# Performance work log

Hardware: AMD Instinct MI355X
Metric: run time of the kernel (lower is better)

Reference implementation:

```python
import jax, jax.numpy as jnp
import numpy as np

B, S, H = 4, 4096, 256
NH, W = 8, 128
DH = H // NH
FF = 1024
NEG = -1e9

def gelu(x):
    return jax.nn.gelu(x, approximate=False)

def layer_norm(x, g, b, eps=1e-9):
    # torch .std() is unbiased (ddof=1); note the (std + eps) denominator, not sqrt(var+eps)
    mean = jnp.mean(x, axis=-1, keepdims=True)
    std = jnp.std(x, axis=-1, keepdims=True, ddof=1)
    return g * (x - mean) / (std + eps) + b

def causal_conv(x, w, b, dilation):
    # x: (B,S,C), w: (9, Cin, Cout); left-padded causal conv (Conv class)
    pad = dilation * 8
    y = jax.lax.conv_general_dilated(x, w, window_strides=(1,), padding=[(pad, 0)],
                                     rhs_dilation=(dilation,), dimension_numbers=('NWC', 'WIO', 'NWC'))
    return y + b

def sliding_window_attention(q, k, v, bias):
    # q,k,v: (B,NH,S,DH); q pre-scaled. Faithful to Longformer sliding_chunks_matmul_qk/pv:
    # band of 2W+1 relative offsets per query, out-of-range keys masked to -inf before softmax.
    b, h, s, d = q.shape
    c = s // W  # number of length-W query chunks
    qc = q.reshape(b, h, c, W, d)
    kp = jnp.pad(k, ((0, 0), (0, 0), (W, W), (0, 0)))
    vp = jnp.pad(v, ((0, 0), (0, 0), (W, W), (0, 0)))
    kidx = (jnp.arange(c) * W)[:, None] + jnp.arange(3 * W)[None, :]  # (c,3W) overlapping key chunks
    kc = kp[:, :, kidx, :]  # (b,h,c,3W,d)
    vc = vp[:, :, kidx, :]
    scores = jnp.einsum('bhcxd,bhcyd->bhcxy', qc, kc)  # (b,h,c,W,3W)
    x = jnp.arange(W)
    r = jnp.arange(2 * W + 1)
    band_idx = x[:, None] + r[None, :]  # (W,2W+1), values in [0,3W-1]
    band = jnp.take_along_axis(scores, band_idx[None, None, None], axis=-1)  # (b,h,c,W,2W+1)
    i = jnp.arange(s).reshape(c, W)
    j = i[:, :, None] + (r - W)[None, None, :]  # global key index per band entry
    valid = (j >= 0) & (j < s)
    band = jnp.where(valid[None, None], band + bias, NEG)  # relative bias depends only on offset
    probs = jax.nn.softmax(band.astype(jnp.float32), axis=-1).astype(q.dtype)
    ridx = jnp.arange(3 * W)[None, :] - x[:, None]  # (W,3W) inverse band->chunk map
    vmask = ((ridx >= 0) & (ridx <= 2 * W)).astype(probs.dtype)
    pc = jnp.take_along_axis(probs, jnp.clip(ridx, 0, 2 * W)[None, None, None], axis=-1) * vmask[None, None, None]
    return jnp.einsum('bhcxy,bhcyd->bhcxd', pc, vc).reshape(b, h, s, d)


def setup_inputs() -> dict:
    key = jax.random.key(0)
    ks = jax.random.split(key, 12)
    inputs = jax.random.normal(ks[0], (B, S, H), jnp.float32)
    dw_w = jax.random.normal(ks[1], (9,), jnp.float32) * 0.1   # depthwise (9,1) kernel, 1 channel
    dw_b = jnp.zeros((1,), jnp.float32)
    pw_w = jax.random.normal(ks[2], (3,), jnp.float32) * 0.5   # pointwise 1->3 conv (scalars)
    pw_b = jnp.zeros((3,), jnp.float32)
    Wq = jax.random.normal(ks[3], (H, H), jnp.float32) * 0.02
    Wk = jax.random.normal(ks[4], (H, H), jnp.float32) * 0.02
    Wv = jax.random.normal(ks[5], (H, H), jnp.float32) * 0.02
    Wo = jax.random.normal(ks[6], (H, H), jnp.float32) * 0.02
    rel_bias = jax.random.normal(ks[7], (2 * S,), jnp.float32) * 0.02
    ln1_g = jnp.ones((H,), jnp.float32); ln1_b = jnp.zeros((H,), jnp.float32)
    ln2_g = jnp.ones((H,), jnp.float32); ln2_b = jnp.zeros((H,), jnp.float32)
    w1 = jax.random.normal(ks[8], (9, H, FF), jnp.float32) * 0.02
    b1 = jnp.zeros((FF,), jnp.float32)
    w2 = jax.random.normal(ks[9], (9, FF, H), jnp.float32) * 0.02
    b2 = jnp.zeros((H,), jnp.float32)
    return {"inputs": inputs, "dw_w": dw_w, "dw_b": dw_b, "pw_w": pw_w, "pw_b": pw_b,
            "Wq": Wq, "Wk": Wk, "Wv": Wv, "Wo": Wo, "rel_bias": rel_bias,
            "ln1_g": ln1_g, "ln1_b": ln1_b, "ln2_g": ln2_g, "ln2_b": ln2_b,
            "w1": w1, "b1": b1, "w2": w2, "b2": b2}


def reference(inputs, dw_w, dw_b, pw_w, pw_b, Wq, Wk, Wv, Wo, rel_bias,
              ln1_g, ln1_b, ln2_g, ln2_b, w1, b1, w2, b2):
    x = inputs
    xn = layer_norm(x, ln1_g, ln1_b)
    # SepConv2d QKV generator: depthwise (9,1) conv along seq (shared over features), GELU,
    # pointwise 1x1 conv 1->3 channels, then GELU again (self.relu in MHA.forward)
    xp = jnp.pad(xn, ((0, 0), (4, 4), (0, 0)))
    dw = jnp.zeros_like(xn)
    for t in range(9):
        dw = dw + dw_w[t] * xp[:, t:t + S, :]
    dw = dw + dw_b[0]
    hmid = gelu(dw)
    qkv = gelu(hmid[None] * pw_w.reshape(3, 1, 1, 1) + pw_b.reshape(3, 1, 1, 1))  # (3,B,S,H)
    q = qkv[0] @ Wq
    k = qkv[1] @ Wk
    v = qkv[2] @ Wv
    split = lambda t: t.reshape(B, S, NH, DH).transpose(0, 2, 1, 3)
    q, k, v = split(q), split(k), split(v)
    q = q * (DH ** -0.5)
    # relative_position_index = arange(2W+1).repeat(lens,1) -> bias uses table[:2W+1] per offset
    bias = rel_bias[:2 * W + 1]
    ctx = sliding_window_attention(q, k, v, bias)
    ctx = ctx.transpose(0, 2, 1, 3).reshape(B, S, H)
    x = x + ctx @ Wo
    xn2 = layer_norm(x, ln2_g, ln2_b)
    # PositionwiseFeedForward 'cc': causal dilated convs; GELU applied after every layer (incl. last)
    f = gelu(causal_conv(xn2, w1, b1, 1))
    f = gelu(causal_conv(f, w2, b2, 8))
    return x + f
```

## Files before the change

### kernel.cpp

```cpp
#include <hip/hip_runtime.h>
#include <stdint.h>

typedef uint16_t u16;
typedef uint32_t u32;

typedef __attribute__((ext_vector_type(8))) short bf16x8;
typedef __attribute__((ext_vector_type(4))) float f32x4;

typedef __attribute__((address_space(1))) const u32 gas_u32;
typedef __attribute__((address_space(3))) u32 las_u32;

#define S_LEN 4096
#define HDIM  256
#define FFDIM 1024

__device__ __forceinline__ float bf2f(u16 u) { return __uint_as_float(((u32)u) << 16); }
__device__ __forceinline__ u16 f2bf(float f) {
  u32 x = __float_as_uint(f);
  return (u16)((x + 0x7fffu + ((x >> 16) & 1u)) >> 16);
}
__device__ __forceinline__ float gelu_f(float x) {
  return 0.5f * x * (1.0f + erff(x * 0.7071067811865475f));
}
__device__ __forceinline__ void glds16(const u16* g, u16* l) {
  __builtin_amdgcn_global_load_lds((gas_u32*)g, (las_u32*)l, 16, 0, 0);
}

__global__ __launch_bounds__(256) void front_kernel(
    const float* __restrict__ Wq, const float* __restrict__ Wk, const float* __restrict__ Wv,
    const float* __restrict__ Wo, const float* __restrict__ W1, const float* __restrict__ W2,
    u16* __restrict__ WqT, u16* __restrict__ WkT, u16* __restrict__ WvT,
    u16* __restrict__ WoT, u16* __restrict__ W1T, u16* __restrict__ W2T, float qscale,
    const float* __restrict__ X, u16* __restrict__ gq, u16* __restrict__ gk, u16* __restrict__ gv,
    const float* __restrict__ ln1g, const float* __restrict__ ln1b,
    const float* __restrict__ dw_w, const float* __restrict__ dw_b,
    const float* __restrict__ pw_w, const float* __restrict__ pw_b) {
  __shared__ u16 t[32][33];
  __shared__ float xnl[24 * 256];
  const int bid = blockIdx.x;
  const int tid = threadIdx.x;
  if (bid < 4864) {
    const float* in; u16* out; int K, N; float scale = 1.0f; int idx;
    if (bid < 256) {
      K = 256; N = 256; idx = bid & 63;
      const int w = bid >> 6;
      in = (w == 0) ? Wq : (w == 1) ? Wk : (w == 2) ? Wv : Wo;
      out = (w == 0) ? WqT : (w == 1) ? WkT : (w == 2) ? WvT : WoT;
      if (w == 0) scale = qscale;
    } else if (bid < 2560) {
      K = 2304; N = 1024; idx = bid - 256; in = W1; out = W1T;
    } else {
      K = 9216; N = 256; idx = bid - 2560; in = W2; out = W2T;
    }
    const int kt = K >> 5;
    const int k0 = (idx % kt) * 32, n0 = (idx / kt) * 32;
    const int tx = tid & 31, ty = tid >> 5;
#pragma unroll
    for (int i = ty; i < 32; i += 8) t[i][tx] = f2bf(in[(long)(k0 + i) * N + (n0 + tx)] * scale);
    __syncthreads();
#pragma unroll
    for (int i = ty; i < 32; i += 8) out[(long)(n0 + i) * K + (k0 + tx)] = t[tx][i];
    return;
  }
  const int ro = (bid - 4864) * 16;
  const int seg_lo = ro & ~(S_LEN - 1);
  const int lane = tid & 63;
  const int ri = tid >> 6;
  const int c0 = lane * 4;
#pragma unroll
  for (int p = 0; p < 6; ++p) {
    const int h = ro - 4 + p * 4 + ri;
    float y[4] = {0.f, 0.f, 0.f, 0.f};
    if (h >= seg_lo && h < seg_lo + S_LEN) {
      float4 f = *(const float4*)(X + (long)h * HDIM + c0);
      float v[4] = {f.x, f.y, f.z, f.w};
      float s = v[0] + v[1] + v[2] + v[3];
#pragma unroll
      for (int o = 32; o > 0; o >>= 1) s += __shfl_xor(s, o);
      const float mean = s * (1.0f / 256.0f);
      float ss = 0.f;
#pragma unroll
      for (int j = 0; j < 4; ++j) { float d = v[j] - mean; ss += d * d; }
#pragma unroll
      for (int o = 32; o > 0; o >>= 1) ss += __shfl_xor(ss, o);
      const float inv_ = 1.0f / (sqrtf(ss * (1.0f / 255.0f)) + 1e-9f);
#pragma unroll
      for (int j = 0; j < 4; ++j) y[j] = ln1g[c0 + j] * (v[j] - mean) * inv_ + ln1b[c0 + j];
    }
    float4 o_; o_.x = y[0]; o_.y = y[1]; o_.z = y[2]; o_.w = y[3];
    *(float4*)&xnl[(p * 4 + ri) * 256 + c0] = o_;
  }
  __syncthreads();
  const float b0 = dw_b[0];
  float wv[9];
#pragma unroll
  for (int q = 0; q < 9; ++q) wv[q] = dw_w[q];
  const float pwv[3] = {pw_w[0], pw_w[1], pw_w[2]};
  const float pbv[3] = {pw_b[0], pw_b[1], pw_b[2]};
  u16* outs[3] = {gq, gk, gv};
#pragma unroll
  for (int p = 0; p < 4; ++p) {
    const int lrow = p * 4 + ri;
    float a0 = b0, a1 = b0, a2 = b0, a3 = b0;
#pragma unroll
    for (int q = 0; q < 9; ++q) {
      const float w = wv[q];
      float4 xv = *(const float4*)&xnl[(lrow + q) * 256 + c0];
      a0 = fmaf(w, xv.x, a0); a1 = fmaf(w, xv.y, a1);
      a2 = fmaf(w, xv.z, a2); a3 = fmaf(w, xv.w, a3);
    }
    float h[4];
    h[0] = gelu_f(a0); h[1] = gelu_f(a1); h[2] = gelu_f(a2); h[3] = gelu_f(a3);
    const long orow = (long)(ro + lrow);
#pragma unroll
    for (int pp = 0; pp < 3; ++pp) {
      float y[4];
#pragma unroll
      for (int j = 0; j < 4; ++j) y[j] = gelu_f(fmaf(h[j], pwv[pp], pbv[pp]));
      uint2 o_;
      o_.x = (u32)f2bf(y[0]) | ((u32)f2bf(y[1]) << 16);
      o_.y = (u32)f2bf(y[2]) | ((u32)f2bf(y[3]) << 16);
      *(uint2*)(outs[pp] + orow * HDIM + c0) = o_;
    }
  }
}

__global__ __launch_bounds__(256) void ln2_kernel(const float* __restrict__ inv, u16* __restrict__ outv,
                                                  const float* __restrict__ g, const float* __restrict__ bsh,
                                                  uint4* __restrict__ gx, uint4* __restrict__ gf) {
  const int tid = threadIdx.x;
  if (blockIdx.x >= 4096) {
    int t = (blockIdx.x - 4096) * 256 + tid;
    const uint4 z = {0u, 0u, 0u, 0u};
    if (t < 1024) {
      const int s = t >> 8, o = t & 255;
      gx[(long)s * 131328 + o] = z;
    } else {
      t -= 1024;
      if (t < 32768) {
        const int s = t >> 13, o = t & 8191;
        gf[(long)s * 532480 + o] = z;
      }
    }
    return;
  }
  const int lane = tid & 63;
  const long row = (long)blockIdx.x * 4 + (tid >> 6);
  const int c0 = lane * 4;
  float v[4];
  float4 f = *(const float4*)(inv + row * HDIM + c0);
  v[0] = f.x; v[1] = f.y; v[2] = f.z; v[3] = f.w;
  float s = v[0] + v[1] + v[2] + v[3];
#pragma unroll
  for (int o = 32; o > 0; o >>= 1) s += __shfl_xor(s, o);
  const float mean = s * (1.0f / 256.0f);
  float ss = 0.f;
#pragma unroll
  for (int j = 0; j < 4; ++j) { float d = v[j] - mean; ss += d * d; }
#pragma unroll
  for (int o = 32; o > 0; o >>= 1) ss += __shfl_xor(ss, o);
  const float inv_ = 1.0f / (sqrtf(ss * (1.0f / 255.0f)) + 1e-9f);
  float y[4];
#pragma unroll
  for (int j = 0; j < 4; ++j) y[j] = g[c0 + j] * (v[j] - mean) * inv_ + bsh[c0 + j];
  const long orow = (row >> 12) * 4104 + 8 + (row & (S_LEN - 1));
  uint2 o_;
  o_.x = (u32)f2bf(y[0]) | ((u32)f2bf(y[1]) << 16);
  o_.y = (u32)f2bf(y[2]) | ((u32)f2bf(y[3]) << 16);
  *(uint2*)(outv + orow * HDIM + c0) = o_;
}

__global__ __launch_bounds__(256) void gemm_qkv(
    const u16* __restrict__ A, const u16* __restrict__ BT, u16* __restrict__ Outv,
    u16* __restrict__ vt, int KW, int N, long a_z, long b_z, long o_z) {
  __shared__ __align__(16) u16 As[128 * 64];
  __shared__ __align__(16) u16 Bs[128 * 64];
  const int tid = threadIdx.x;
  const int lane = tid & 63;
  const int wid = tid >> 6;
  const int wm = (wid & 1) * 64;
  const int wn = (wid >> 1) * 64;
  const int fm = lane & 15;
  const int fq = lane >> 4;
  const int t0 = blockIdx.x * 128;
  const int n0 = blockIdx.y * 128;
  A += (long)blockIdx.z * a_z;
  BT += (long)blockIdx.z * b_z;

  const int srow = lane >> 3;
  const int cseg = (((lane & 7) ^ srow) << 3);

  f32x4 acc[4][4];
#pragma unroll
  for (int a = 0; a < 4; ++a)
#pragma unroll
    for (int b = 0; b < 4; ++b) acc[a][b] = (f32x4){0.f, 0.f, 0.f, 0.f};

  u16* alb = &As[wid * 32 * 64];
  u16* blb = &Bs[wid * 32 * 64];

  for (int k0 = 0; k0 < KW; k0 += 64) {
    const u16* ag = A + (long)(t0 + wid * 32 + srow) * KW + k0 + cseg;
    const u16* bg = BT + (long)(n0 + wid * 32 + srow) * KW + k0 + cseg;
#pragma unroll
    for (int j = 0; j < 4; ++j) {
      glds16(ag + (long)(8 * j) * KW, alb + j * 8 * 64);
      glds16(bg + (long)(8 * j) * KW, blb + j * 8 * 64);
    }
    __syncthreads();
#pragma unroll
    for (int kk = 0; kk < 2; ++kk) {
      const int g = kk * 4 + fq;
      const u16* ap = &As[(wm + fm) * 64 + ((g ^ (fm & 7)) << 3)];
      const u16* bp = &Bs[(wn + fm) * 64 + ((g ^ (fm & 7)) << 3)];
      bf16x8 af[4], bfv[4];
#pragma unroll
      for (int t = 0; t < 4; ++t) {
        af[t] = *(const bf16x8*)(ap + t * 1024);
        bfv[t] = *(const bf16x8*)(bp + t * 1024);
      }
#pragma unroll
      for (int mi = 0; mi < 4; ++mi)
#pragma unroll
        for (int ni = 0; ni < 4; ++ni)
          acc[mi][ni] = __builtin_amdgcn_mfma_f32_16x16x32_bf16(af[mi], bfv[ni], acc[mi][ni], 0, 0, 0);
    }
    __syncthreads();
  }

#pragma unroll
  for (int mi = 0; mi < 4; ++mi)
#pragma unroll
    for (int ni = 0; ni < 4; ++ni) {
      if (blockIdx.z == 2) {
        const int col = n0 + wn + ni * 16 + fm;
        const int hh = col >> 5, dd = col & 31;
        const long trow0 = t0 + wm + mi * 16 + fq * 4;
        const long bb = trow0 >> 12;
        const int s0 = (int)(trow0 & (S_LEN - 1));
        uint2 o_;
        o_.x = (u32)f2bf(acc[mi][ni][0]) | ((u32)f2bf(acc[mi][ni][1]) << 16);
        o_.y = (u32)f2bf(acc[mi][ni][2]) | ((u32)f2bf(acc[mi][ni][3]) << 16);
        *(uint2*)(vt + ((bb * 8 + hh) * 32 + dd) * S_LEN + s0) = o_;
      } else {
#pragma unroll
        for (int r = 0; r < 4; ++r) {
          const long trow = t0 + wm + mi * 16 + fq * 4 + r;
          const int col = n0 + wn + ni * 16 + fm;
          (Outv + (long)blockIdx.z * o_z)[trow * N + col] = f2bf(acc[mi][ni][r]);
        }
      }
    }
}

__global__ __launch_bounds__(256) void gemm_wo(
    const u16* __restrict__ A, const u16* __restrict__ BT, float* __restrict__ Outv,
    const float* __restrict__ residv, int KW, int N) {
  __shared__ __align__(16) u16 As[128 * 64];
  __shared__ __align__(16) u16 Bs[128 * 64];
  const int tid = threadIdx.x;
  const int lane = tid & 63;
  const int wid = tid >> 6;
  const int wm = (wid & 1) * 64;
  const int wn = (wid >> 1) * 64;
  const int fm = lane & 15;
  const int fq = lane >> 4;
  const int t0 = blockIdx.x * 128;
  const int n0 = blockIdx.y * 128;

  const int srow = lane >> 3;
  const int cseg = (((lane & 7) ^ srow) << 3);

  f32x4 acc[4][4];
#pragma unroll
  for (int a = 0; a < 4; ++a)
#pragma unroll
    for (int b = 0; b < 4; ++b) acc[a][b] = (f32x4){0.f, 0.f, 0.f, 0.f};

  u16* alb = &As[wid * 32 * 64];
  u16* blb = &Bs[wid * 32 * 64];

  for (int k0 = 0; k0 < KW; k0 += 64) {
    const u16* ag = A + (long)(t0 + wid * 32 + srow) * KW + k0 + cseg;
    const u16* bg = BT + (long)(n0 + wid * 32 + srow) * KW + k0 + cseg;
#pragma unroll
    for (int j = 0; j < 4; ++j) {
      glds16(ag + (long)(8 * j) * KW, alb + j * 8 * 64);
      glds16(bg + (long)(8 * j) * KW, blb + j * 8 * 64);
    }
    __syncthreads();
#pragma unroll
    for (int kk = 0; kk < 2; ++kk) {
      const int g = kk * 4 + fq;
      const u16* ap = &As[(wm + fm) * 64 + ((g ^ (fm & 7)) << 3)];
      const u16* bp = &Bs[(wn + fm) * 64 + ((g ^ (fm & 7)) << 3)];
      bf16x8 af[4], bfv[4];
#pragma unroll
      for (int t = 0; t < 4; ++t) {
        af[t] = *(const bf16x8*)(ap + t * 1024);
        bfv[t] = *(const bf16x8*)(bp + t * 1024);
      }
#pragma unroll
      for (int mi = 0; mi < 4; ++mi)
#pragma unroll
        for (int ni = 0; ni < 4; ++ni)
          acc[mi][ni] = __builtin_amdgcn_mfma_f32_16x16x32_bf16(af[mi], bfv[ni], acc[mi][ni], 0, 0, 0);
    }
    __syncthreads();
  }

#pragma unroll
  for (int mi = 0; mi < 4; ++mi)
#pragma unroll
    for (int ni = 0; ni < 4; ++ni)
#pragma unroll
      for (int r = 0; r < 4; ++r) {
        const long trow = t0 + wm + mi * 16 + fq * 4 + r;
        const int col = n0 + wn + ni * 16 + fm;
        Outv[trow * N + col] = acc[mi][ni][r] + residv[trow * N + col];
      }
}

__global__ __launch_bounds__(256) void attn_mfma(const u16* __restrict__ Q, const u16* __restrict__ K,
                                                 const u16* __restrict__ VT, const float* __restrict__ rel,
                                                 u16* __restrict__ CTX) {
  __shared__ __align__(16) u16 Ks[384 * 36];
  __shared__ __align__(16) u16 VTs[32 * 388];
  __shared__ __align__(16) u16 Ps[4][32 * 72];
  __shared__ float bias_s[260];
  const int c = blockIdx.x, h = blockIdx.y, b = blockIdx.z;
  const int tid = threadIdx.x;
  const int lane = tid & 63, wid = tid >> 6;
  const int fm = lane & 15, fq = lane >> 4;
  const int j0 = c * 128 - 128;
  const long kvbase = ((long)b * S_LEN) * HDIM + h * 32;
  const long vtbase = (((long)b * 8 + h) * 32) * S_LEN;

  for (int idx = tid; idx < 384 * 4; idx += 256) {
    const int jj = idx >> 2, seg = (idx & 3) * 8;
    int j = j0 + jj; j = j < 0 ? 0 : (j > S_LEN - 1 ? S_LEN - 1 : j);
    uint4 kv = *(const uint4*)(K + kvbase + (long)j * HDIM + seg);
    *(uint4*)&Ks[jj * 36 + seg] = kv;
  }
#pragma unroll
  for (int p = 0; p < 6; ++p) {
    const int idx = p * 256 + tid;
    const int d = idx / 48, seg = idx - d * 48;
    int off = j0 + seg * 8; off = off < 0 ? 0 : (off > S_LEN - 8 ? S_LEN - 8 : off);
    uint4 vv = *(const uint4*)(VT + vtbase + (long)d * S_LEN + off);
    *(uint4*)&VTs[d * 388 + seg * 8] = vv;
  }
  for (int idx = tid; idx < 257; idx += 256) bias_s[idx] = rel[idx];
  __syncthreads();

  bf16x8 aq[2];
#pragma unroll
  for (int mi = 0; mi < 2; ++mi)
    aq[mi] = *(const bf16x8*)(Q + kvbase + (long)(c * 128 + wid * 32 + mi * 16 + fm) * HDIM + fq * 8);

  const int klo = (c == 0) ? 128 : 0;
  const int khi = (c == 31) ? 255 : 383;

  float m_r[2][4], l_r[2][4];
  f32x4 acc[2][2];
#pragma unroll
  for (int mi = 0; mi < 2; ++mi)
#pragma unroll
    for (int r = 0; r < 4; ++r) { m_r[mi][r] = -1e9f; l_r[mi][r] = 0.f; }
#pragma unroll
  for (int mi = 0; mi < 2; ++mi)
#pragma unroll
    for (int nd = 0; nd < 2; ++nd) acc[mi][nd] = (f32x4){0.f, 0.f, 0.f, 0.f};

  u16* pw = &Ps[wid][0];

  for (int ch = 0; ch < 6; ++ch) {
    f32x4 sc[2][4];
#pragma unroll
    for (int ni = 0; ni < 4; ++ni) {
      bf16x8 bk = *(const bf16x8*)&Ks[(ch * 64 + ni * 16 + fm) * 36 + fq * 8];
#pragma unroll
      for (int mi = 0; mi < 2; ++mi)
        sc[mi][ni] = __builtin_amdgcn_mfma_f32_16x16x32_bf16(aq[mi], bk, (f32x4){0.f, 0.f, 0.f, 0.f}, 0, 0, 0);
    }
    float cm[2][4];
#pragma unroll
    for (int mi = 0; mi < 2; ++mi)
#pragma unroll
      for (int r = 0; r < 4; ++r) cm[mi][r] = -1e9f;
#pragma unroll
    for (int mi = 0; mi < 2; ++mi)
#pragma unroll
      for (int ni = 0; ni < 4; ++ni) {
        const int keyloc = ch * 64 + ni * 16 + fm;
        const bool kval = (keyloc >= klo) && (keyloc <= khi);
#pragma unroll
        for (int r = 0; r < 4; ++r) {
          const int qloc = wid * 32 + mi * 16 + fq * 4 + r;
          const int rr = keyloc - qloc;
          const bool valid = kval && (rr >= 0) && (rr <= 256);
          const int rc = valid ? rr : 0;
          float vv = sc[mi][ni][r] + bias_s[rc];
          vv = valid ? vv : -1e9f;
          sc[mi][ni][r] = vv;
          cm[mi][r] = fmaxf(cm[mi][r], vv);
        }
      }
#pragma unroll
    for (int mi = 0; mi < 2; ++mi)
#pragma unroll
      for (int r = 0; r < 4; ++r) {
        float x = cm[mi][r];
        x = fmaxf(x, __shfl_xor(x, 1));
        x = fmaxf(x, __shfl_xor(x, 2));
        x = fmaxf(x, __shfl_xor(x, 4));
        x = fmaxf(x, __shfl_xor(x, 8));
        cm[mi][r] = x;
      }
    float alpha[2][4];
#pragma unroll
    for (int mi = 0; mi < 2; ++mi)
#pragma unroll
      for (int r = 0; r < 4; ++r) {
        const float nm = fmaxf(m_r[mi][r], cm[mi][r]);
        alpha[mi][r] = __expf(m_r[mi][r] - nm);
        m_r[mi][r] = nm;
        l_r[mi][r] *= alpha[mi][r];
      }
#pragma unroll
    for (int mi = 0; mi < 2; ++mi)
#pragma unroll
      for (int nd = 0; nd < 2; ++nd)
#pragma unroll
        for (int r = 0; r < 4; ++r) acc[mi][nd][r] *= alpha[mi][r];
#pragma unroll
    for (int mi = 0; mi < 2; ++mi)
#pragma unroll
      for (int ni = 0; ni < 4; ++ni)
#pragma unroll
        for (int r = 0; r < 4; ++r) {
          const float pv = __expf(sc[mi][ni][r] - m_r[mi][r]);
          l_r[mi][r] += pv;
          pw[(mi * 16 + fq * 4 + r) * 72 + ni * 16 + fm] = f2bf(pv);
        }
#pragma unroll
    for (int kc = 0; kc < 2; ++kc) {
      bf16x8 ap[2], bv[2];
#pragma unroll
      for (int mi = 0; mi < 2; ++mi)
        ap[mi] = *(const bf16x8*)&pw[(mi * 16 + fm) * 72 + kc * 32 + fq * 8];
#pragma unroll
      for (int nd = 0; nd < 2; ++nd)
        bv[nd] = *(const bf16x8*)&VTs[(nd * 16 + fm) * 388 + ch * 64 + kc * 32 + fq * 8];
#pragma unroll
      for (int mi = 0; mi < 2; ++mi)
#pragma unroll
        for (int nd = 0; nd < 2; ++nd)
          acc[mi][nd] = __builtin_amdgcn_mfma_f32_16x16x32_bf16(ap[mi], bv[nd], acc[mi][nd], 0, 0, 0);
    }
  }

  float linv[2][4];
#pragma unroll
  for (int mi = 0; mi < 2; ++mi)
#pragma unroll
    for (int r = 0; r < 4; ++r) {
      float x = l_r[mi][r];
      x += __shfl_xor(x, 1);
      x += __shfl_xor(x, 2);
      x += __shfl_xor(x, 4);
      x += __shfl_xor(x, 8);
      linv[mi][r] = 1.0f / x;
    }
#pragma unroll
  for (int mi = 0; mi < 2; ++mi)
#pragma unroll
    for (int nd = 0; nd < 2; ++nd)
#pragma unroll
      for (int r = 0; r < 4; ++r) {
        const long s = c * 128 + wid * 32 + mi * 16 + fq * 4 + r;
        CTX[((long)b * S_LEN + s) * HDIM + h * 32 + nd * 16 + fm] = f2bf(acc[mi][nd][r] * linv[mi][r]);
      }
}

template <int APITCH, int NTAPS, int DIL, int NN>
__global__ __launch_bounds__(256, 2) void gemm_conv(
    const u16* __restrict__ Apad, const u16* __restrict__ BT, void* __restrict__ Outv,
    const float* __restrict__ bias,
    int SEGR, int BPITCH, int OSEGR, int OGUARD) {
  constexpr int AROWS = 256 + (NTAPS - 1) * DIL;
  constexpr int AOPS = (AROWS + 7) / 8;
  __shared__ __align__(16) u16 As[AOPS * 8 * 64];
  __shared__ __align__(16) u16 Bs2[2][128 * 64];
  const int tid = threadIdx.x;
  const int lane = tid & 63;
  const int wid = tid >> 6;
  const int wm = (wid & 1) * 128;
  const int wn = (wid >> 1) * 64;
  const int fm = lane & 15;
  const int fq = lane >> 4;
  const int t0 = blockIdx.x * 256;
  const int n0 = blockIdx.y * 128;

  const int seg = t0 >> 12;
  const long abase = (long)seg * SEGR + (t0 & (S_LEN - 1));
  const int srow = lane >> 3;
  const int cseg = (((lane & 7) ^ srow) << 3);

  f32x4 acc[8][4];
#pragma unroll
  for (int a = 0; a < 8; ++a)
#pragma unroll
    for (int b = 0; b < 4; ++b) acc[a][b] = (f32x4){0.f, 0.f, 0.f, 0.f};

  for (int k0 = 0; k0 < APITCH; k0 += 64) {
    for (int op = wid; op < AOPS; op += 4)
      glds16(Apad + (abase + op * 8 + srow) * APITCH + k0 + cseg, &As[op * 8 * 64]);
#pragma unroll
    for (int j = 0; j < 4; ++j)
      glds16(BT + (long)(n0 + wid * 32 + j * 8 + srow) * BPITCH + k0 + cseg,
             &Bs2[0][(wid * 32 + j * 8) * 64]);
    __syncthreads();
#pragma unroll
    for (int u = 0; u < NTAPS; ++u) {
      if (u + 1 < NTAPS) {
        const long bc = (long)(u + 1) * APITCH + k0;
#pragma unroll
        for (int j = 0; j < 4; ++j)
          glds16(BT + (long)(n0 + wid * 32 + j * 8 + srow) * BPITCH + bc + cseg,
                 &Bs2[(u + 1) & 1][(wid * 32 + j * 8) * 64]);
      }
      const int du = u * DIL;
      const u16* bsp = Bs2[u & 1];
#pragma unroll
      for (int kk = 0; kk < 2; ++kk) {
        const int g = kk * 4 + fq;
        const u16* ap = &As[(wm + fm + du) * 64 + ((g ^ ((fm + du) & 7)) << 3)];
        const u16* bp = &bsp[(wn + fm) * 64 + ((g ^ (fm & 7)) << 3)];
        bf16x8 af[8], bfv[4];
#pragma unroll
        for (int t = 0; t < 8; ++t) af[t] = *(const bf16x8*)(ap + t * 1024);
#pragma unroll
        for (int t = 0; t < 4; ++t) bfv[t] = *(const bf16x8*)(bp + t * 1024);
#pragma unroll
        for (int mi = 0; mi < 8; ++mi)
#pragma unroll
          for (int ni = 0; ni < 4; ++ni)
            acc[mi][ni] = __builtin_amdgcn_mfma_f32_16x16x32_bf16(af[mi], bfv[ni], acc[mi][ni], 0, 0, 0);
      }
      __syncthreads();
    }
  }

#pragma unroll
  for (int mi = 0; mi < 8; ++mi)
#pragma unroll
    for (int ni = 0; ni < 4; ++ni)
#pragma unroll
      for (int r = 0; r < 4; ++r) {
        const long trow = t0 + wm + mi * 16 + fq * 4 + r;
        const int col = n0 + wn + ni * 16 + fm;
        const long orow = (trow >> 12) * OSEGR + OGUARD + (trow & (S_LEN - 1));
        ((u16*)Outv)[orow * NN + col] = f2bf(gelu_f(acc[mi][ni][r] + bias[col]));
      }
}

__global__ __launch_bounds__(256) void gemm_conv_s(
    const u16* __restrict__ Apad, const u16* __restrict__ BT, u16* __restrict__ Outv,
    int APITCH, int SEGR, int BPITCH, int ntaps, int dil, int N, long out_z_off) {
  __shared__ __align__(16) u16 As[144 * 64];
  __shared__ __align__(16) u16 Bs2[2][128 * 64];
  const int tid = threadIdx.x;
  const int lane = tid & 63;
  const int wid = tid >> 6;
  const int wm = (wid & 1) * 64;
  const int wn = (wid >> 1) * 64;
  const int fm = lane & 15;
  const int fq = lane >> 4;
  const int t0 = blockIdx.x * 128;
  const int n0 = blockIdx.y * 128;
  const int tap0 = blockIdx.z * ntaps;

  const int seg = t0 >> 12;
  const long abase = (long)seg * SEGR + (t0 & (S_LEN - 1)) + (long)tap0 * dil;
  const int aops = (128 + (ntaps - 1) * dil + 7) >> 3;

  const int srow = lane >> 3;
  const int cseg = (((lane & 7) ^ srow) << 3);

  f32x4 acc[4][4];
#pragma unroll
  for (int a = 0; a < 4; ++a)
#pragma unroll
    for (int b = 0; b < 4; ++b) acc[a][b] = (f32x4){0.f, 0.f, 0.f, 0.f};

  for (int k0 = 0; k0 < APITCH; k0 += 64) {
    for (int op = wid; op < aops; op += 4)
      glds16(Apad + (abase + op * 8 + srow) * APITCH + k0 + cseg, &As[op * 8 * 64]);
    {
      const long bc = (long)tap0 * APITCH + k0;
#pragma unroll
      for (int j = 0; j < 4; ++j)
        glds16(BT + (long)(n0 + wid * 32 + j * 8 + srow) * BPITCH + bc + cseg,
               &Bs2[0][(wid * 32 + j * 8) * 64]);
    }
    __syncthreads();
    for (int u = 0; u < ntaps; ++u) {
      if (u + 1 < ntaps) {
        const long bc = (long)(tap0 + u + 1) * APITCH + k0;
#pragma unroll
        for (int j = 0; j < 4; ++j)
          glds16(BT + (long)(n0 + wid * 32 + j * 8 + srow) * BPITCH + bc + cseg,
                 &Bs2[(u + 1) & 1][(wid * 32 + j * 8) * 64]);
      }
      const int du = u * dil;
      const u16* bsp = Bs2[u & 1];
#pragma unroll
      for (int kk = 0; kk < 2; ++kk) {
        const int g = kk * 4 + fq;
        const u16* ap = &As[(wm + fm + du) * 64 + ((g ^ (fm & 7)) << 3)];
        const u16* bp = &bsp[(wn + fm) * 64 + ((g ^ (fm & 7)) << 3)];
        bf16x8 af[4], bfv[4];
#pragma unroll
        for (int t = 0; t < 4; ++t) {
          af[t] = *(const bf16x8*)(ap + t * 1024);
          bfv[t] = *(const bf16x8*)(bp + t * 1024);
        }
#pragma unroll
        for (int mi = 0; mi < 4; ++mi)
#pragma unroll
          for (int ni = 0; ni < 4; ++ni)
            acc[mi][ni] = __builtin_amdgcn_mfma_f32_16x16x32_bf16(af[mi], bfv[ni], acc[mi][ni], 0, 0, 0);
      }
      __syncthreads();
    }
  }

#pragma unroll
  for (int mi = 0; mi < 4; ++mi)
#pragma unroll
    for (int ni = 0; ni < 4; ++ni)
#pragma unroll
      for (int r = 0; r < 4; ++r) {
        const long trow = t0 + wm + mi * 16 + fq * 4 + r;
        const int col = n0 + wn + ni * 16 + fm;
        (Outv + (long)blockIdx.z * out_z_off)[trow * N + col] = f2bf(acc[mi][ni][r]);
      }
}

__global__ __launch_bounds__(256) void final_kernel(const float* __restrict__ x2, const u16* __restrict__ P,
                                                    const float* __restrict__ b2, float* __restrict__ out) {
  const long i4 = ((long)blockIdx.x * 256 + threadIdx.x) * 4;
  const int c0 = (int)(i4 & (HDIM - 1));
  float4 xa = *(const float4*)(x2 + i4);
  uint2 u0 = *(const uint2*)(P + i4);
  uint2 u1 = *(const uint2*)(P + 4194304 + i4);
  uint2 u2 = *(const uint2*)(P + 8388608 + i4);
  float pv[4];
  pv[0] = bf2f((u16)(u0.x & 0xffffu)) + bf2f((u16)(u1.x & 0xffffu)) + bf2f((u16)(u2.x & 0xffffu));
  pv[1] = bf2f((u16)(u0.x >> 16)) + bf2f((u16)(u1.x >> 16)) + bf2f((u16)(u2.x >> 16));
  pv[2] = bf2f((u16)(u0.y & 0xffffu)) + bf2f((u16)(u1.y & 0xffffu)) + bf2f((u16)(u2.y & 0xffffu));
  pv[3] = bf2f((u16)(u0.y >> 16)) + bf2f((u16)(u1.y >> 16)) + bf2f((u16)(u2.y >> 16));
  float4 o_;
  o_.x = xa.x + gelu_f(pv[0] + b2[c0 + 0]);
  o_.y = xa.y + gelu_f(pv[1] + b2[c0 + 1]);
  o_.z = xa.z + gelu_f(pv[2] + b2[c0 + 2]);
  o_.w = xa.w + gelu_f(pv[3] + b2[c0 + 3]);
  *(float4*)(out + i4) = o_;
}

extern "C" void kernel_launch(void* const* d_in, const int* in_sizes, int n_in,
                              void* d_out, int out_size, void* d_ws, size_t ws_size,
                              hipStream_t stream) {
  (void)in_sizes; (void)n_in; (void)out_size;
  const float* X    = (const float*)d_in[0];
  const float* dw_w = (const float*)d_in[1];
  const float* dw_b = (const float*)d_in[2];
  const float* pw_w = (const float*)d_in[3];
  const float* pw_b = (const float*)d_in[4];
  const float* Wq   = (const float*)d_in[5];
  const float* Wk   = (const float*)d_in[6];
  const float* Wv   = (const float*)d_in[7];
  const float* Wo   = (const float*)d_in[8];
  const float* rel  = (const float*)d_in[9];
  const float* ln1g = (const float*)d_in[10];
  const float* ln1b = (const float*)d_in[11];
  const float* ln2g = (const float*)d_in[12];
  const float* ln2b = (const float*)d_in[13];
  const float* w1   = (const float*)d_in[14];
  const float* b1   = (const float*)d_in[15];
  const float* w2   = (const float*)d_in[16];
  const float* b2   = (const float*)d_in[17];

  if (ws_size < 119537664) return;

  char* ws = (char*)d_ws;
  u16* WqT = (u16*)(ws + 0);
  u16* WkT = (u16*)(ws + 131072);
  u16* WvT = (u16*)(ws + 262144);
  u16* WoT = (u16*)(ws + 393216);
  u16* W1T = (u16*)(ws + 524288);
  u16* W2T = (u16*)(ws + 5242880);
  float* x2  = (float*)(ws + 10485760);
  u16* gq  = (u16*)(ws + 27262976);
  u16* gk  = (u16*)(ws + 35651584);
  u16* gv  = (u16*)(ws + 44040192);
  u16* q   = (u16*)(ws + 52428800);
  u16* vt  = (u16*)(ws + 69206016);
  u16* ctx = (u16*)(ws + 77594624);
  u16* f1p  = (u16*)(ws + 27262976);
  u16* xn2p = (u16*)(ws + 61341696);
  u16* P    = (u16*)(ws + 61341696);

  const float qscale = 0.17677669529663687f;
  front_kernel<<<5888, 256, 0, stream>>>(Wq, Wk, Wv, Wo, w1, w2,
      WqT, WkT, WvT, WoT, W1T, W2T, qscale,
      X, gq, gk, gv, ln1g, ln1b, dw_w, dw_b, pw_w, pw_b);

  gemm_qkv<<<dim3(128, 2, 3), 256, 0, stream>>>(gq, WqT, q, vt,
      256, 256, 4194304, 65536, 4194304);

  attn_mfma<<<dim3(32, 8, 4), 256, 0, stream>>>(q, q + 4194304, vt, rel, ctx);

  gemm_wo<<<dim3(128, 2), 256, 0, stream>>>(ctx, WoT, x2, X, 256, 256);

  ln2_kernel<<<4228, 256, 0, stream>>>(x2, xn2p, ln2g, ln2b, (uint4*)xn2p, (uint4*)f1p);

  gemm_conv<256, 9, 1, 1024><<<dim3(64, 8), 256, 0, stream>>>(
      xn2p, W1T, f1p, b1, 4104, 2304, 4160, 64);

  gemm_conv_s<<<dim3(128, 2, 3), 256, 0, stream>>>(f1p, W2T, P,
      1024, 4160, 9216, 3, 8, 256, 4194304);

  final_kernel<<<4096, 256, 0, stream>>>(x2, P, b2, (float*)d_out);
}
```

Baseline: 381.8 us.

## Prepack conv weights in MFMA fragment order and stream B straight to registers

The front kernel now packs W1 and W2 into bf16 tiles already laid out as MFMA B-fragments, replacing the plain transposes. A new unified conv GEMM loads those fragments from global memory into registers with a one-iteration prefetch and double-buffers only the A tile in LDS, so B no longer goes through LDS. The second conv moves from a tap split with 128-row tiles to an input-channel split-K (4 partials) with 256-row tiles, and the final kernel now sums four partials. This aims to cut LDS traffic and barriers in the FFN GEMMs. In exchange it adds register pressure and extra partial-sum memory traffic.

Measured after the change: 385.2 us. About the same (+0.9%).

```diff
diff --git a/kernel.cpp b/kernel.cpp
--- a/kernel.cpp
+++ b/kernel.cpp
@@ -30,7 +30,7 @@
     const float* __restrict__ Wq, const float* __restrict__ Wk, const float* __restrict__ Wv,
     const float* __restrict__ Wo, const float* __restrict__ W1, const float* __restrict__ W2,
     u16* __restrict__ WqT, u16* __restrict__ WkT, u16* __restrict__ WvT,
-    u16* __restrict__ WoT, u16* __restrict__ W1T, u16* __restrict__ W2T, float qscale,
+    u16* __restrict__ WoT, u16* __restrict__ W1F, u16* __restrict__ W2F, float qscale,
     const float* __restrict__ X, u16* __restrict__ gq, u16* __restrict__ gk, u16* __restrict__ gv,
     const float* __restrict__ ln1g, const float* __restrict__ ln1b,
     const float* __restrict__ dw_w, const float* __restrict__ dw_b,
@@ -39,30 +39,48 @@
   __shared__ float xnl[24 * 256];
   const int bid = blockIdx.x;
   const int tid = threadIdx.x;
-  if (bid < 4864) {
-    const float* in; u16* out; int K, N; float scale = 1.0f; int idx;
-    if (bid < 256) {
-      K = 256; N = 256; idx = bid & 63;
-      const int w = bid >> 6;
-      in = (w == 0) ? Wq : (w == 1) ? Wk : (w == 2) ? Wv : Wo;
-      out = (w == 0) ? WqT : (w == 1) ? WkT : (w == 2) ? WvT : WoT;
-      if (w == 0) scale = qscale;
-    } else if (bid < 2560) {
-      K = 2304; N = 1024; idx = bid - 256; in = W1; out = W1T;
-    } else {
-      K = 9216; N = 256; idx = bid - 2560; in = W2; out = W2T;
-    }
-    const int kt = K >> 5;
-    const int k0 = (idx % kt) * 32, n0 = (idx / kt) * 32;
+  if (bid < 256) {
+    const int idx = bid & 63;
+    const int w = bid >> 6;
+    const float* in = (w == 0) ? Wq : (w == 1) ? Wk : (w == 2) ? Wv : Wo;
+    u16* out = (w == 0) ? WqT : (w == 1) ? WkT : (w == 2) ? WvT : WoT;
+    const float scale = (w == 0) ? qscale : 1.0f;
+    const int k0 = (idx & 7) * 32, n0 = (idx >> 3) * 32;
     const int tx = tid & 31, ty = tid >> 5;
 #pragma unroll
-    for (int i = ty; i < 32; i += 8) t[i][tx] = f2bf(in[(long)(k0 + i) * N + (n0 + tx)] * scale);
+    for (int i = ty; i < 32; i += 8) t[i][tx] = f2bf(in[(long)(k0 + i) * 256 + (n0 + tx)] * scale);
     __syncthreads();
 #pragma unroll
-    for (int i = ty; i < 32; i += 8) out[(long)(n0 + i) * K + (k0 + tx)] = t[tx][i];
+    for (int i = ty; i < 32; i += 8) out[(long)(n0 + i) * 256 + (k0 + tx)] = t[tx][i];
     return;
   }
-  const int ro = (bid - 4864) * 16;
+  if (bid < 1408) {
+    const int isC2 = bid >= 832;
+    const int idx = bid - (isC2 ? 832 : 256);
+    const float* w = isC2 ? W2 : W1;
+    u16* dst = isC2 ? W2F : W1F;
+    const int AP = isC2 ? 1024 : 256;
+    const int NNl = isC2 ? 256 : 1024;
+    const int per_n = (AP / 64) * 9;
+    const int n64g = idx / per_n;
+    const int r = idx - n64g * per_n;
+    const int k0i = r / 9, u = r - k0i * 9;
+    const long pktbase = (((long)n64g * (AP / 64) + k0i) * 9 + u) * 2;
+    for (int g = tid; g < 512; g += 256) {
+      const int kk = g >> 8, rr = g & 255, tt = rr >> 6, ln = rr & 63;
+      const int n = n64g * 64 + tt * 16 + (ln & 15);
+      const int kin = k0i * 64 + kk * 32 + (ln >> 4) * 8;
+      const float* src = w + (long)(u * AP + kin) * NNl + n;
+      u32 p0 = (u32)f2bf(src[0]) | ((u32)f2bf(src[(long)NNl]) << 16);
+      u32 p1 = (u32)f2bf(src[2l * NNl]) | ((u32)f2bf(src[3l * NNl]) << 16);
+      u32 p2 = (u32)f2bf(src[4l * NNl]) | ((u32)f2bf(src[5l * NNl]) << 16);
+      u32 p3 = (u32)f2bf(src[6l * NNl]) | ((u32)f2bf(src[7l * NNl]) << 16);
+      uint4 pk; pk.x = p0; pk.y = p1; pk.z = p2; pk.w = p3;
+      *(uint4*)(dst + (pktbase + kk) * 2048 + (long)(tt * 64 + ln) * 8) = pk;
+    }
+    return;
+  }
+  const int ro = (bid - 1408) * 16;
   const int seg_lo = ro & ~(S_LEN - 1);
   const int lane = tid & 63;
   const int ri = tid >> 6;
@@ -483,29 +501,25 @@
       }
 }
 
-template <int APITCH, int NTAPS, int DIL, int NN>
-__global__ __launch_bounds__(256, 2) void gemm_conv(
-    const u16* __restrict__ Apad, const u16* __restrict__ BT, void* __restrict__ Outv,
-    const float* __restrict__ bias,
-    int SEGR, int BPITCH, int OSEGR, int OGUARD) {
-  constexpr int AROWS = 256 + (NTAPS - 1) * DIL;
+template <int EPI, int APITCH, int DIL, int NN, int K0PERZ>
+__global__ __launch_bounds__(256, 2) void gemm_convB(
+    const u16* __restrict__ Apad, const u16* __restrict__ Bpk, void* __restrict__ Outv,
+    const float* __restrict__ bias, int SEGR, int OSEGR, int OGUARD, long out_z_off) {
+  constexpr int K0 = APITCH / 64;
+  constexpr int AROWS = 256 + 8 * DIL;
   constexpr int AOPS = (AROWS + 7) / 8;
-  __shared__ __align__(16) u16 As[AOPS * 8 * 64];
-  __shared__ __align__(16) u16 Bs2[2][128 * 64];
-  const int tid = threadIdx.x;
-  const int lane = tid & 63;
-  const int wid = tid >> 6;
-  const int wm = (wid & 1) * 128;
-  const int wn = (wid >> 1) * 64;
-  const int fm = lane & 15;
-  const int fq = lane >> 4;
-  const int t0 = blockIdx.x * 256;
-  const int n0 = blockIdx.y * 128;
-
+  __shared__ __align__(16) u16 As[2][AOPS * 8 * 64];
+  const int tid = threadIdx.x, lane = tid & 63, wid = tid >> 6;
+  const int wm = (wid & 1) * 128, wn = (wid >> 1) * 64;
+  const int fm = lane & 15, fq = lane >> 4;
+  const int t0 = blockIdx.x * 256, n0 = blockIdx.y * 128;
+  const int zz = blockIdx.z;
+  const int k0base = zz * K0PERZ;
   const int seg = t0 >> 12;
   const long abase = (long)seg * SEGR + (t0 & (S_LEN - 1));
   const int srow = lane >> 3;
   const int cseg = (((lane & 7) ^ srow) << 3);
+  const long n64g = (n0 + wn) >> 6;
 
   f32x4 acc[8][4];
 #pragma unroll
@@ -513,44 +527,67 @@
 #pragma unroll
     for (int b = 0; b < 4; ++b) acc[a][b] = (f32x4){0.f, 0.f, 0.f, 0.f};
 
-  for (int k0 = 0; k0 < APITCH; k0 += 64) {
-    for (int op = wid; op < AOPS; op += 4)
-      glds16(Apad + (abase + op * 8 + srow) * APITCH + k0 + cseg, &As[op * 8 * 64]);
-#pragma unroll
-    for (int j = 0; j < 4; ++j)
-      glds16(BT + (long)(n0 + wid * 32 + j * 8 + srow) * BPITCH + k0 + cseg,
-             &Bs2[0][(wid * 32 + j * 8) * 64]);
-    __syncthreads();
-#pragma unroll
-    for (int u = 0; u < NTAPS; ++u) {
-      if (u + 1 < NTAPS) {
-        const long bc = (long)(u + 1) * APITCH + k0;
-#pragma unroll
-        for (int j = 0; j < 4; ++j)
-          glds16(BT + (long)(n0 + wid * 32 + j * 8 + srow) * BPITCH + bc + cseg,
-                 &Bs2[(u + 1) & 1][(wid * 32 + j * 8) * 64]);
-      }
-      const int du = u * DIL;
-      const u16* bsp = Bs2[u & 1];
-#pragma unroll
-      for (int kk = 0; kk < 2; ++kk) {
-        const int g = kk * 4 + fq;
-        const u16* ap = &As[(wm + fm + du) * 64 + ((g ^ ((fm + du) & 7)) << 3)];
-        const u16* bp = &bsp[(wn + fm) * 64 + ((g ^ (fm & 7)) << 3)];
-        bf16x8 af[8], bfv[4];
-#pragma unroll
-        for (int t = 0; t < 8; ++t) af[t] = *(const bf16x8*)(ap + t * 1024);
-#pragma unroll
-        for (int t = 0; t < 4; ++t) bfv[t] = *(const bf16x8*)(bp + t * 1024);
-#pragma unroll
-        for (int mi = 0; mi < 8; ++mi)
-#pragma unroll
-          for (int ni = 0; ni < 4; ++ni)
-            acc[mi][ni] = __builtin_amdgcn_mfma_f32_16x16x32_bf16(af[mi], bfv[ni], acc[mi][ni], 0, 0, 0);
-      }
-      __syncthreads();
-    }
-  }
+#define STAGE_A(k0i, buf)                                                              \
+  {                                                                                    \
+    const int kc_ = (k0base + (k0i)) * 64;                                             \
+    for (int op = wid; op < AOPS; op += 4)                                             \
+      glds16(Apad + (abase + op * 8 + srow) * APITCH + kc_ + cseg, &As[(buf)][op * 8 * 64]); \
+  }
+
+#define LOAD_B(it, dst)                                                                \
+  {                                                                                    \
+    const int k0i_ = (it) / 9, u_ = (it) - k0i_ * 9;                                   \
+    const u16* pb_ = Bpk + (((n64g * K0 + (k0base + k0i_)) * 9 + u_) * 2) * 2048 + (long)lane * 8; \
+    _Pragma("unroll")                                                                  \
+    for (int kk_ = 0; kk_ < 2; ++kk_)                                                  \
+      _Pragma("unroll")                                                                \
+      for (int t_ = 0; t_ < 4; ++t_)                                                   \
+        dst[kk_ * 4 + t_] = *(const bf16x8*)(pb_ + kk_ * 2048 + t_ * 512);             \
+  }
+
+#define MFMA_TAP(u, buf, br)                                                           \
+  {                                                                                    \
+    const int du_ = (u) * DIL;                                                         \
+    _Pragma("unroll")                                                                  \
+    for (int kk_ = 0; kk_ < 2; ++kk_) {                                                \
+      const int g_ = kk_ * 4 + fq;                                                     \
+      const u16* ap_ = &As[(buf)][(wm + fm + du_) * 64 + ((g_ ^ ((fm + du_) & 7)) << 3)]; \
+      bf16x8 af_[8];                                                                   \
+      _Pragma("unroll")                                                                \
+      for (int t_ = 0; t_ < 8; ++t_) af_[t_] = *(const bf16x8*)(ap_ + t_ * 1024);      \
+      _Pragma("unroll")                                                                \
+      for (int mi_ = 0; mi_ < 8; ++mi_)                                                \
+        _Pragma("unroll")                                                              \
+        for (int ni_ = 0; ni_ < 4; ++ni_)                                              \
+          acc[mi_][ni_] = __builtin_amdgcn_mfma_f32_16x16x32_bf16(af_[mi_], br[kk_ * 4 + ni_], acc[mi_][ni_], 0, 0, 0); \
+    }                                                                                  \
+  }
+
+  constexpr int NIT = K0PERZ * 9;
+  bf16x8 br0[8], br1[8];
+  STAGE_A(0, 0);
+  LOAD_B(0, br0);
+  __syncthreads();
+  for (int it = 0; it < NIT; it += 2) {
+    {
+      const int k0i = it / 9, u = it - k0i * 9;
+      if (it + 1 < NIT) LOAD_B(it + 1, br1);
+      if (u == 1 && k0i + 1 < K0PERZ) STAGE_A(k0i + 1, (k0i + 1) & 1);
+      MFMA_TAP(u, k0i & 1, br0);
+      if (u == 8) __syncthreads();
+    }
+    {
+      const int it2 = it + 1;
+      const int k0i = it2 / 9, u = it2 - k0i * 9;
+      if (it2 + 1 < NIT) LOAD_B(it2 + 1, br0);
+      if (u == 1 && k0i + 1 < K0PERZ) STAGE_A(k0i + 1, (k0i + 1) & 1);
+      MFMA_TAP(u, k0i & 1, br1);
+      if (u == 8) __syncthreads();
+    }
+  }
+#undef STAGE_A
+#undef LOAD_B
+#undef MFMA_TAP
 
 #pragma unroll
   for (int mi = 0; mi < 8; ++mi)
@@ -560,91 +597,13 @@
       for (int r = 0; r < 4; ++r) {
         const long trow = t0 + wm + mi * 16 + fq * 4 + r;
         const int col = n0 + wn + ni * 16 + fm;
-        const long orow = (trow >> 12) * OSEGR + OGUARD + (trow & (S_LEN - 1));
-        ((u16*)Outv)[orow * NN + col] = f2bf(gelu_f(acc[mi][ni][r] + bias[col]));
-      }
-}
-
-__global__ __launch_bounds__(256) void gemm_conv_s(
-    const u16* __restrict__ Apad, const u16* __restrict__ BT, u16* __restrict__ Outv,
-    int APITCH, int SEGR, int BPITCH, int ntaps, int dil, int N, long out_z_off) {
-  __shared__ __align__(16) u16 As[144 * 64];
-  __shared__ __align__(16) u16 Bs2[2][128 * 64];
-  const int tid = threadIdx.x;
-  const int lane = tid & 63;
-  const int wid = tid >> 6;
-  const int wm = (wid & 1) * 64;
-  const int wn = (wid >> 1) * 64;
-  const int fm = lane & 15;
-  const int fq = lane >> 4;
-  const int t0 = blockIdx.x * 128;
-  const int n0 = blockIdx.y * 128;
-  const int tap0 = blockIdx.z * ntaps;
-
-  const int seg = t0 >> 12;
-  const long abase = (long)seg * SEGR + (t0 & (S_LEN - 1)) + (long)tap0 * dil;
-  const int aops = (128 + (ntaps - 1) * dil + 7) >> 3;
-
-  const int srow = lane >> 3;
-  const int cseg = (((lane & 7) ^ srow) << 3);
-
-  f32x4 acc[4][4];
-#pragma unroll
-  for (int a = 0; a < 4; ++a)
-#pragma unroll
-    for (int b = 0; b < 4; ++b) acc[a][b] = (f32x4){0.f, 0.f, 0.f, 0.f};
-
-  for (int k0 = 0; k0 < APITCH; k0 += 64) {
-    for (int op = wid; op < aops; op += 4)
-      glds16(Apad + (abase + op * 8 + srow) * APITCH + k0 + cseg, &As[op * 8 * 64]);
-    {
-      const long bc = (long)tap0 * APITCH + k0;
-#pragma unroll
-      for (int j = 0; j < 4; ++j)
-        glds16(BT + (long)(n0 + wid * 32 + j * 8 + srow) * BPITCH + bc + cseg,
-               &Bs2[0][(wid * 32 + j * 8) * 64]);
-    }
-    __syncthreads();
-    for (int u = 0; u < ntaps; ++u) {
-      if (u + 1 < ntaps) {
-        const long bc = (long)(tap0 + u + 1) * APITCH + k0;
-#pragma unroll
-        for (int j = 0; j < 4; ++j)
-          glds16(BT + (long)(n0 + wid * 32 + j * 8 + srow) * BPITCH + bc + cseg,
-                 &Bs2[(u + 1) & 1][(wid * 32 + j * 8) * 64]);
-      }
-      const int du = u * dil;
-      const u16* bsp = Bs2[u & 1];
-#pragma unroll
-      for (int kk = 0; kk < 2; ++kk) {
-        const int g = kk * 4 + fq;
-        const u16* ap = &As[(wm + fm + du) * 64 + ((g ^ (fm & 7)) << 3)];
-        const u16* bp = &bsp[(wn + fm) * 64 + ((g ^ (fm & 7)) << 3)];
-        bf16x8 af[4], bfv[4];
-#pragma unroll
-        for (int t = 0; t < 4; ++t) {
-          af[t] = *(const bf16x8*)(ap + t * 1024);
-          bfv[t] = *(const bf16x8*)(bp + t * 1024);
+        const float cv = acc[mi][ni][r];
+        if (EPI == 2) {
+          const long orow = (trow >> 12) * OSEGR + OGUARD + (trow & (S_LEN - 1));
+          ((u16*)Outv)[orow * NN + col] = f2bf(gelu_f(cv + bias[col]));
+        } else {
+          ((u16*)Outv + (long)zz * out_z_off)[trow * NN + col] = f2bf(cv);
         }
-#pragma unroll
-        for (int mi = 0; mi < 4; ++mi)
-#pragma unroll
-          for (int ni = 0; ni < 4; ++ni)
-            acc[mi][ni] = __builtin_amdgcn_mfma_f32_16x16x32_bf16(af[mi], bfv[ni], acc[mi][ni], 0, 0, 0);
-      }
-      __syncthreads();
-    }
-  }
-
-#pragma unroll
-  for (int mi = 0; mi < 4; ++mi)
-#pragma unroll
-    for (int ni = 0; ni < 4; ++ni)
-#pragma unroll
-      for (int r = 0; r < 4; ++r) {
-        const long trow = t0 + wm + mi * 16 + fq * 4 + r;
-        const int col = n0 + wn + ni * 16 + fm;
-        (Outv + (long)blockIdx.z * out_z_off)[trow * N + col] = f2bf(acc[mi][ni][r]);
       }
 }
 
@@ -656,11 +615,12 @@
   uint2 u0 = *(const uint2*)(P + i4);
   uint2 u1 = *(const uint2*)(P + 4194304 + i4);
   uint2 u2 = *(const uint2*)(P + 8388608 + i4);
+  uint2 u3 = *(const uint2*)(P + 12582912 + i4);
   float pv[4];
-  pv[0] = bf2f((u16)(u0.x & 0xffffu)) + bf2f((u16)(u1.x & 0xffffu)) + bf2f((u16)(u2.x & 0xffffu));
-  pv[1] = bf2f((u16)(u0.x >> 16)) + bf2f((u16)(u1.x >> 16)) + bf2f((u16)(u2.x >> 16));
-  pv[2] = bf2f((u16)(u0.y & 0xffffu)) + bf2f((u16)(u1.y & 0xffffu)) + bf2f((u16)(u2.y & 0xffffu));
-  pv[3] = bf2f((u16)(u0.y >> 16)) + bf2f((u16)(u1.y >> 16)) + bf2f((u16)(u2.y >> 16));
+  pv[0] = bf2f((u16)(u0.x & 0xffffu)) + bf2f((u16)(u1.x & 0xffffu)) + bf2f((u16)(u2.x & 0xffffu)) + bf2f((u16)(u3.x & 0xffffu));
+  pv[1] = bf2f((u16)(u0.x >> 16)) + bf2f((u16)(u1.x >> 16)) + bf2f((u16)(u2.x >> 16)) + bf2f((u16)(u3.x >> 16));
+  pv[2] = bf2f((u16)(u0.y & 0xffffu)) + bf2f((u16)(u1.y & 0xffffu)) + bf2f((u16)(u2.y & 0xffffu)) + bf2f((u16)(u3.y & 0xffffu));
+  pv[3] = bf2f((u16)(u0.y >> 16)) + bf2f((u16)(u1.y >> 16)) + bf2f((u16)(u2.y >> 16)) + bf2f((u16)(u3.y >> 16));
   float4 o_;
   o_.x = xa.x + gelu_f(pv[0] + b2[c0 + 0]);
   o_.y = xa.y + gelu_f(pv[1] + b2[c0 + 1]);
@@ -699,8 +659,8 @@
   u16* WkT = (u16*)(ws + 131072);
   u16* WvT = (u16*)(ws + 262144);
   u16* WoT = (u16*)(ws + 393216);
-  u16* W1T = (u16*)(ws + 524288);
-  u16* W2T = (u16*)(ws + 5242880);
+  u16* W1F = (u16*)(ws + 524288);
+  u16* W2F = (u16*)(ws + 5242880);
   float* x2  = (float*)(ws + 10485760);
   u16* gq  = (u16*)(ws + 27262976);
   u16* gk  = (u16*)(ws + 35651584);
@@ -713,8 +673,8 @@
   u16* P    = (u16*)(ws + 61341696);
 
   const float qscale = 0.17677669529663687f;
-  front_kernel<<<5888, 256, 0, stream>>>(Wq, Wk, Wv, Wo, w1, w2,
-      WqT, WkT, WvT, WoT, W1T, W2T, qscale,
+  front_kernel<<<2432, 256, 0, stream>>>(Wq, Wk, Wv, Wo, w1, w2,
+      WqT, WkT, WvT, WoT, W1F, W2F, qscale,
       X, gq, gk, gv, ln1g, ln1b, dw_w, dw_b, pw_w, pw_b);
 
   gemm_qkv<<<dim3(128, 2, 3), 256, 0, stream>>>(gq, WqT, q, vt,
@@ -726,11 +686,11 @@
 
   ln2_kernel<<<4228, 256, 0, stream>>>(x2, xn2p, ln2g, ln2b, (uint4*)xn2p, (uint4*)f1p);
 
-  gemm_conv<256, 9, 1, 1024><<<dim3(64, 8), 256, 0, stream>>>(
-      xn2p, W1T, f1p, b1, 4104, 2304, 4160, 64);
-
-  gemm_conv_s<<<dim3(128, 2, 3), 256, 0, stream>>>(f1p, W2T, P,
-      1024, 4160, 9216, 3, 8, 256, 4194304);
+  gemm_convB<2, 256, 1, 1024, 4><<<dim3(64, 8, 1), 256, 0, stream>>>(
+      xn2p, W1F, f1p, b1, 4104, 4160, 64, 0);
+
+  gemm_convB<3, 1024, 8, 256, 4><<<dim3(64, 2, 4), 256, 0, stream>>>(
+      f1p, W2F, P, nullptr, 4160, 0, 0, 4194304);
 
   final_kernel<<<4096, 256, 0, stream>>>(x2, P, b2, (float*)d_out);
 }
```
